# Optimization experiments

Measured on AMD Instinct MI355X. Metric: run time of the kernel, lower is better.

Reference implementation:

```python
import jax, jax.numpy as jnp
import numpy as np

N_NODES = 1_000_000
HIDDEN = 64
N_LAYERS = 4
N_ORB = 16                      # dim_h = N_ORB**2, dim_g = N_ORB**4
DIM_H = N_ORB * N_ORB
DIM_G = N_ORB ** 4
INV_SQRT_H = 1.0 / np.sqrt(HIDDEN).astype(np.float32)

# 8-fold permutation symmetry of real two-electron integrals (ij|kl)
G_PERMS = [(0, 1, 2, 3), (1, 0, 2, 3), (0, 1, 3, 2), (1, 0, 3, 2),
           (2, 3, 0, 1), (3, 2, 0, 1), (2, 3, 1, 0), (3, 2, 1, 0)]


def setup_inputs() -> dict:
    key = jax.random.key(0)
    ks = jax.random.split(key, 9)
    return {
        "Z": jax.random.randint(ks[0], (N_NODES,), 0, 120, dtype=jnp.int64),
        "pos": jax.random.normal(ks[1], (N_NODES, 3), dtype=jnp.float32),
        "ghost": jax.random.randint(ks[2], (N_NODES,), 0, 2, dtype=jnp.int32),
        "embed": jax.random.normal(ks[3], (120, HIDDEN), dtype=jnp.float32),
        "W_tp": jax.random.normal(ks[4], (N_LAYERS, HIDDEN, HIDDEN), dtype=jnp.float32) * INV_SQRT_H,
        "w_h": jax.random.normal(ks[5], (HIDDEN, DIM_H), dtype=jnp.float32) * INV_SQRT_H,
        "b_h": jax.random.normal(ks[6], (DIM_H,), dtype=jnp.float32),
        "w_g": jax.random.normal(ks[7], (HIDDEN, DIM_G), dtype=jnp.float32) * INV_SQRT_H,
        "b_g": jax.random.normal(ks[8], (DIM_G,), dtype=jnp.float32),
    }


def reference(Z, pos, ghost, embed, W_tp, w_h, b_h, w_g, b_g):
    # Node embedding gather: [N, H]
    x = embed[Z]

    # FullyConnectedTensorProduct output irreps is '0e', only the 0e x 0e -> 0e
    # CG path survives; Y0 is a constant (component normalization => 1.0).
    y0 = jnp.float32(1.0)

    for l in range(N_LAYERS):
        # tensor-product layer collapsed to its sole scalar CG path + Gate (silu)
        x = jax.nn.silu((x @ W_tp[l]) * (y0 * INV_SQRT_H))

    # Global sum pool over nodes -> [H]
    g_feat = x.sum(axis=0)

    h = g_feat @ w_h + b_h            # [DIM_H]
    g = g_feat @ w_g + b_g            # [DIM_G]

    # symmetrize_h: h -> (h + h^T)/2 as an N_ORB x N_ORB matrix
    hm = h.reshape(N_ORB, N_ORB)
    hm = 0.5 * (hm + hm.T)

    # symmetrize_g: average over the 8 permutation symmetries of (ij|kl)
    gm = g.reshape(N_ORB, N_ORB, N_ORB, N_ORB)
    gm = sum(jnp.transpose(gm, p) for p in G_PERMS) / jnp.float32(len(G_PERMS))

    return jnp.concatenate([hm.reshape(-1), gm.reshape(-1)], axis=-1)
```

## Files before the change

### kernel.cpp

```cpp
#include <hip/hip_runtime.h>

#define HIDDEN 64
#define NLAYERS 4
#define NZ 120
#define NZP 128
#define DIM_H 256
#define DIM_G 65536
#define NB_HIST 256
#define NB_G 256
#define MAGIC 0x5F3C0D1Eu
#define SPIN_CAP 300000

#define B_MLP0 NB_HIST
#define B_G0   (NB_HIST + NZ)
#define B_AGG  (B_G0 + NB_G)
#define NBLK   (B_AGG + 1)

#define WS_PFLAG   0
#define WS_TFLAG   1024
#define WS_GFFLAG  1536
#define WS_SYMFLAG 1600
#define WS_GFLAG   2048
#define WS_PART    4096
#define WS_TAB     135168
#define WS_GF      165888
#define WS_GRAW    169984

#define IDX4(a,bb,c,d) ((((a)*16+(bb))*16+(c))*16+(d))

__device__ inline unsigned aload(const unsigned* p) {
    return __hip_atomic_load(p, __ATOMIC_RELAXED, __HIP_MEMORY_SCOPE_AGENT);
}
__device__ inline void astore(unsigned* p, unsigned v) {
    __hip_atomic_store(p, v, __ATOMIC_RELAXED, __HIP_MEMORY_SCOPE_AGENT);
}
__device__ inline float aloadf(const float* p) {
    return __hip_atomic_load(p, __ATOMIC_RELAXED, __HIP_MEMORY_SCOPE_AGENT);
}
__device__ inline void astoref(float* p, float v) {
    __hip_atomic_store(p, v, __ATOMIC_RELAXED, __HIP_MEMORY_SCOPE_AGENT);
}

__device__ inline void poll1(const unsigned* flag, int sleep_sel) {
    for (int it = 0; it < SPIN_CAP; ++it) {
        unsigned v = 0;
        if ((threadIdx.x & 63) == 0) v = aload(flag);
        v = (unsigned)__shfl((int)v, 0, 64);
        if (v == MAGIC) break;
        if (sleep_sel == 0) __builtin_amdgcn_s_sleep(16);
        else                __builtin_amdgcn_s_sleep(32);
    }
}

__global__ void __launch_bounds__(256, 3) k_fused(
        const int* __restrict__ Z, int n,
        const float* __restrict__ embed, const float* __restrict__ Wtp,
        const float* __restrict__ w_h, const float* __restrict__ b_h,
        const float* __restrict__ w_g, const float* __restrict__ b_g,
        unsigned* pflag, unsigned* tflag, unsigned* gfflag, unsigned* symflag,
        unsigned* gflag, unsigned* part, float* table, float* gfbuf, float* graw,
        float* __restrict__ out)
{
    const int b = blockIdx.x, t = threadIdx.x;

    if (b < NB_HIST) {
        __shared__ unsigned hist[NZP];
        for (int i = t; i < NZP; i += 256) hist[i] = 0;
        int lane = t & 63;
        bool is64 = (__ballot(Z[2 * lane + 1] != 0) == 0ULL);
        __syncthreads();
        const int stride = NB_HIST * 256 * 4;
        for (int base = (b * 256 + t) * 4; base < n; base += stride) {
            if (base + 3 < n) {
                int v0, v1, v2, v3;
                if (!is64) {
                    int4 q4 = *(const int4*)(Z + base);
                    v0 = q4.x; v1 = q4.y; v2 = q4.z; v3 = q4.w;
                } else {
                    int4 a4 = *(const int4*)(Z + 2 * base);
                    int4 c4 = *(const int4*)(Z + 2 * base + 4);
                    v0 = a4.x; v1 = a4.z; v2 = c4.x; v3 = c4.z;
                }
                atomicAdd(&hist[min(max(v0, 0), NZ - 1)], 1u);
                atomicAdd(&hist[min(max(v1, 0), NZ - 1)], 1u);
                atomicAdd(&hist[min(max(v2, 0), NZ - 1)], 1u);
                atomicAdd(&hist[min(max(v3, 0), NZ - 1)], 1u);
            } else {
                for (int e = base; e < n; ++e) {
                    int v = is64 ? Z[2 * e] : Z[e];
                    atomicAdd(&hist[min(max(v, 0), NZ - 1)], 1u);
                }
            }
        }
        __syncthreads();
        if (t < NZP) astore(&part[b * NZP + t], hist[t]);
        __syncthreads();
        if (t == 0) astore(&pflag[b], MAGIC);

        poll1(symflag, 1);
        int q = b * 256 + t;
        int l = q & 15, k = (q >> 4) & 15, j = (q >> 8) & 15, i = (q >> 12) & 15;
        float s = aloadf(&graw[IDX4(i,j,k,l)]) + aloadf(&graw[IDX4(j,i,k,l)])
                + aloadf(&graw[IDX4(i,j,l,k)]) + aloadf(&graw[IDX4(j,i,l,k)])
                + aloadf(&graw[IDX4(k,l,i,j)]) + aloadf(&graw[IDX4(l,k,i,j)])
                + aloadf(&graw[IDX4(k,l,j,i)]) + aloadf(&graw[IDX4(l,k,j,i)]);
        out[DIM_H + q] = s * 0.125f;

    } else if (b < B_G0) {
        int z = b - B_MLP0;
        if (t < 64) {
            int c = t;
            float x = embed[z * HIDDEN + c];
            for (int l = 0; l < NLAYERS; ++l) {
                const float* W = Wtp + l * HIDDEN * HIDDEN;
                float u = 0.f;
                #pragma unroll
                for (int k = 0; k < HIDDEN; ++k) u += __shfl(x, k, 64) * W[k * HIDDEN + c];
                u *= 0.125f;
                x = u / (1.f + expf(-u));
            }
            astoref(&table[z * HIDDEN + c], x);
        }
        __syncthreads();
        if (t == 0) astore(&tflag[z], MAGIC);

    } else if (b < B_AGG) {
        int i = b - B_G0;
        int p = i * 256 + t;
        float w[HIDDEN];
        #pragma unroll
        for (int c = 0; c < HIDDEN; ++c) w[c] = w_g[c * DIM_G + p];
        float bg = b_g[p];

        poll1(gfflag, 0);
        __shared__ float gfl[HIDDEN];
        if (t < HIDDEN) gfl[t] = aloadf(&gfbuf[t]);
        __syncthreads();
        float acc = bg;
        #pragma unroll
        for (int c = 0; c < HIDDEN; ++c) acc += gfl[c] * w[c];
        astoref(&graw[p], acc);
        __syncthreads();
        if (t == 0) astore(&gflag[i], MAGIC);

    } else {
        for (int it = 0; it < SPIN_CAP; ++it) {
            int ok = 1;
            if (t < NB_HIST) ok &= (aload(&pflag[t]) == MAGIC);
            if (t < NZ)      ok &= (aload(&tflag[t]) == MAGIC);
            if (__syncthreads_and(ok)) break;
            __builtin_amdgcn_s_sleep(8);
        }
        __shared__ float psum[256];
        __shared__ float cnt_s[NZP];
        __shared__ float gfp[4 * HIDDEN];
        __shared__ float gfl[HIDDEN];
        {
            int bin = t & 127, half = t >> 7;
            unsigned s = 0;
            #pragma unroll 8
            for (int r = 0; r < NB_HIST / 2; ++r)
                s += aload(&part[(half * (NB_HIST / 2) + r) * NZP + bin]);
            psum[t] = (float)s;
        }
        __syncthreads();
        if (t < NZP) cnt_s[t] = psum[t] + psum[t + 128];
        __syncthreads();
        {
            int c = t & 63, zg = t >> 6;
            float s = 0.f;
            #pragma unroll
            for (int zz = 0; zz < 30; ++zz) {
                int z = zg * 30 + zz;
                s += cnt_s[z] * aloadf(&table[z * HIDDEN + c]);
            }
            gfp[zg * HIDDEN + c] = s;
        }
        __syncthreads();
        if (t < HIDDEN) {
            float g = gfp[t] + gfp[HIDDEN + t] + gfp[2 * HIDDEN + t] + gfp[3 * HIDDEN + t];
            gfl[t] = g;
            astoref(&gfbuf[t], g);
        }
        __syncthreads();
        if (t == 0) astore(gfflag, MAGIC);

        __shared__ float hbuf[DIM_H];
        float a = b_h[t];
        #pragma unroll
        for (int c = 0; c < HIDDEN; ++c) a += gfl[c] * w_h[c * DIM_H + t];
        hbuf[t] = a;
        __syncthreads();
        out[t] = 0.5f * (hbuf[t] + hbuf[(t & 15) * 16 + (t >> 4)]);

        for (int it = 0; it < SPIN_CAP; ++it) {
            int ok = (t < NB_G) ? (aload(&gflag[t]) == MAGIC) : 1;
            if (__syncthreads_and(ok)) break;
            __builtin_amdgcn_s_sleep(8);
        }
        if (t == 0) astore(symflag, MAGIC);
    }
}

extern "C" void kernel_launch(void* const* d_in, const int* in_sizes, int n_in,
                              void* d_out, int out_size, void* d_ws, size_t ws_size,
                              hipStream_t stream) {
    const int*   Z     = (const int*)  d_in[0];
    const float* embed = (const float*)d_in[3];
    const float* Wtp   = (const float*)d_in[4];
    const float* w_h   = (const float*)d_in[5];
    const float* b_h   = (const float*)d_in[6];
    const float* w_g   = (const float*)d_in[7];
    const float* b_g   = (const float*)d_in[8];
    float* out = (float*)d_out;

    int n = in_sizes[0];

    char* ws = (char*)d_ws;
    unsigned* pflag   = (unsigned*)(ws + WS_PFLAG);
    unsigned* tflag   = (unsigned*)(ws + WS_TFLAG);
    unsigned* gfflag  = (unsigned*)(ws + WS_GFFLAG);
    unsigned* symflag = (unsigned*)(ws + WS_SYMFLAG);
    unsigned* gflag   = (unsigned*)(ws + WS_GFLAG);
    unsigned* part    = (unsigned*)(ws + WS_PART);
    float*    table   = (float*)   (ws + WS_TAB);
    float*    gfbuf   = (float*)   (ws + WS_GF);
    float*    graw    = (float*)   (ws + WS_GRAW);

    k_fused<<<NBLK, 256, 0, stream>>>(Z, n, embed, Wtp, w_h, b_h, w_g, b_g,
                                      pflag, tflag, gfflag, symflag, gflag,
                                      part, table, gfbuf, graw, out);
}
```

Baseline: 16.15 us.

## Spread histogram partial reduction across MLP blocks and shorten spin sleeps

Moves the reduction of the 256 per-block histogram partials out of the single aggregator block and into 16 of the MLP-table blocks. Each of these sums 8 bins with a warp shuffle reduction and then publishes counts plus a completion flag. The aggregator now waits only on these 16 flags and the table flags, which takes a serial reduction off the critical path. Spin-wait sleeps are cut to the minimum for faster wakeup, at the cost of more polling traffic. Extra syncthreads are added after the polls so the shared-memory reads follow the flag check across the whole block.

```diff
diff --git a/kernel.cpp b/kernel.cpp
--- a/kernel.cpp
+++ b/kernel.cpp
@@ -8,6 +8,7 @@
 #define DIM_G 65536
 #define NB_HIST 256
 #define NB_G 256
+#define NB_RED 16
 #define MAGIC 0x5F3C0D1Eu
 #define SPIN_CAP 300000
 
@@ -18,9 +19,11 @@
 
 #define WS_PFLAG   0
 #define WS_TFLAG   1024
-#define WS_GFFLAG  1536
-#define WS_SYMFLAG 1600
+#define WS_CFLAG   1536
+#define WS_GFFLAG  1664
+#define WS_SYMFLAG 1728
 #define WS_GFLAG   2048
+#define WS_CNT     3072
 #define WS_PART    4096
 #define WS_TAB     135168
 #define WS_GF      165888
@@ -41,14 +44,13 @@
     __hip_atomic_store(p, v, __ATOMIC_RELAXED, __HIP_MEMORY_SCOPE_AGENT);
 }
 
-__device__ inline void poll1(const unsigned* flag, int sleep_sel) {
+__device__ inline void poll1(const unsigned* flag) {
     for (int it = 0; it < SPIN_CAP; ++it) {
         unsigned v = 0;
         if ((threadIdx.x & 63) == 0) v = aload(flag);
         v = (unsigned)__shfl((int)v, 0, 64);
         if (v == MAGIC) break;
-        if (sleep_sel == 0) __builtin_amdgcn_s_sleep(16);
-        else                __builtin_amdgcn_s_sleep(32);
+        __builtin_amdgcn_s_sleep(1);
     }
 }
 
@@ -57,9 +59,9 @@
         const float* __restrict__ embed, const float* __restrict__ Wtp,
         const float* __restrict__ w_h, const float* __restrict__ b_h,
         const float* __restrict__ w_g, const float* __restrict__ b_g,
-        unsigned* pflag, unsigned* tflag, unsigned* gfflag, unsigned* symflag,
-        unsigned* gflag, unsigned* part, float* table, float* gfbuf, float* graw,
-        float* __restrict__ out)
+        unsigned* pflag, unsigned* tflag, unsigned* cflag, unsigned* gfflag,
+        unsigned* symflag, unsigned* gflag, unsigned* part, unsigned* cnt,
+        float* table, float* gfbuf, float* graw, float* __restrict__ out)
 {
     const int b = blockIdx.x, t = threadIdx.x;
 
@@ -97,7 +99,8 @@
         __syncthreads();
         if (t == 0) astore(&pflag[b], MAGIC);
 
-        poll1(symflag, 1);
+        poll1(symflag);
+        __syncthreads();
         int q = b * 256 + t;
         int l = q & 15, k = (q >> 4) & 15, j = (q >> 8) & 15, i = (q >> 12) & 15;
         float s = aloadf(&graw[IDX4(i,j,k,l)]) + aloadf(&graw[IDX4(j,i,k,l)])
@@ -124,6 +127,26 @@
         __syncthreads();
         if (t == 0) astore(&tflag[z], MAGIC);
 
+        if (z < NB_RED) {
+            for (int it = 0; it < SPIN_CAP; ++it) {
+                int ok = (aload(&pflag[t]) == MAGIC);
+                if (__syncthreads_and(ok)) break;
+                __builtin_amdgcn_s_sleep(1);
+            }
+            int bin = z * 8 + (t >> 5);
+            int chunk = t & 31;
+            unsigned s = 0;
+            #pragma unroll
+            for (int r = 0; r < 8; ++r)
+                s += aload(&part[(chunk * 8 + r) * NZP + bin]);
+            #pragma unroll
+            for (int off = 16; off > 0; off >>= 1)
+                s += (unsigned)__shfl_down((int)s, off, 32);
+            if (chunk == 0) astore(&cnt[bin], s);
+            __syncthreads();
+            if (t == 0) astore(&cflag[z], MAGIC);
+        }
+
     } else if (b < B_AGG) {
         int i = b - B_G0;
         int p = i * 256 + t;
@@ -132,8 +155,9 @@
         for (int c = 0; c < HIDDEN; ++c) w[c] = w_g[c * DIM_G + p];
         float bg = b_g[p];
 
-        poll1(gfflag, 0);
+        poll1(gfflag);
         __shared__ float gfl[HIDDEN];
+        __syncthreads();
         if (t < HIDDEN) gfl[t] = aloadf(&gfbuf[t]);
         __syncthreads();
         float acc = bg;
@@ -146,25 +170,15 @@
     } else {
         for (int it = 0; it < SPIN_CAP; ++it) {
             int ok = 1;
-            if (t < NB_HIST) ok &= (aload(&pflag[t]) == MAGIC);
-            if (t < NZ)      ok &= (aload(&tflag[t]) == MAGIC);
+            if (t < NB_RED) ok &= (aload(&cflag[t]) == MAGIC);
+            if (t < NZ)     ok &= (aload(&tflag[t]) == MAGIC);
             if (__syncthreads_and(ok)) break;
-            __builtin_amdgcn_s_sleep(8);
-        }
-        __shared__ float psum[256];
+            __builtin_amdgcn_s_sleep(1);
+        }
         __shared__ float cnt_s[NZP];
         __shared__ float gfp[4 * HIDDEN];
         __shared__ float gfl[HIDDEN];
-        {
-            int bin = t & 127, half = t >> 7;
-            unsigned s = 0;
-            #pragma unroll 8
-            for (int r = 0; r < NB_HIST / 2; ++r)
-                s += aload(&part[(half * (NB_HIST / 2) + r) * NZP + bin]);
-            psum[t] = (float)s;
-        }
-        __syncthreads();
-        if (t < NZP) cnt_s[t] = psum[t] + psum[t + 128];
+        if (t < NZP) cnt_s[t] = (float)aload(&cnt[t]);
         __syncthreads();
         {
             int c = t & 63, zg = t >> 6;
@@ -196,7 +210,7 @@
         for (int it = 0; it < SPIN_CAP; ++it) {
             int ok = (t < NB_G) ? (aload(&gflag[t]) == MAGIC) : 1;
             if (__syncthreads_and(ok)) break;
-            __builtin_amdgcn_s_sleep(8);
+            __builtin_amdgcn_s_sleep(1);
         }
         if (t == 0) astore(symflag, MAGIC);
     }
@@ -219,15 +233,17 @@
     char* ws = (char*)d_ws;
     unsigned* pflag   = (unsigned*)(ws + WS_PFLAG);
     unsigned* tflag   = (unsigned*)(ws + WS_TFLAG);
+    unsigned* cflag   = (unsigned*)(ws + WS_CFLAG);
     unsigned* gfflag  = (unsigned*)(ws + WS_GFFLAG);
     unsigned* symflag = (unsigned*)(ws + WS_SYMFLAG);
     unsigned* gflag   = (unsigned*)(ws + WS_GFLAG);
     unsigned* part    = (unsigned*)(ws + WS_PART);
+    unsigned* cnt     = (unsigned*)(ws + WS_CNT);
     float*    table   = (float*)   (ws + WS_TAB);
     float*    gfbuf   = (float*)   (ws + WS_GF);
     float*    graw    = (float*)   (ws + WS_GRAW);
 
     k_fused<<<NBLK, 256, 0, stream>>>(Z, n, embed, Wtp, w_h, b_h, w_g, b_g,
-                                      pflag, tflag, gfflag, symflag, gflag,
-                                      part, table, gfbuf, graw, out);
-}
+                                      pflag, tflag, cflag, gfflag, symflag, gflag,
+                                      part, cnt, table, gfbuf, graw, out);
+}
```

After: 17.47 us. 1.08x slower.
